# Optimization experiments

Measured on AMD Instinct MI355X. Metric: run time of the kernel, lower is better.

Reference implementation:

```python
import jax, jax.numpy as jnp
import numpy as np

N_NODES = 50000
N_EDGES = 800000
INPUT_DIM = 8
HIDDEN_DIM = 128


def setup_inputs() -> dict:
    key = jax.random.key(0)
    k = jax.random.split(key, 8)
    x = jax.random.normal(k[0], (N_NODES, INPUT_DIM), dtype=jnp.float32)
    edge_index = jax.random.randint(k[1], (2, N_EDGES), 0, N_NODES, dtype=jnp.int64)
    edge_attr = jax.random.uniform(k[2], (N_EDGES, 1), dtype=jnp.float32)
    node_embedding = jax.random.normal(k[3], (N_NODES, HIDDEN_DIM), dtype=jnp.float32)
    # Linear weights stored as [in, out] so y = x @ W (bias=False everywhere)
    s1 = 1.0 / np.sqrt(INPUT_DIM)
    sh = 1.0 / np.sqrt(HIDDEN_DIM)
    W1 = jax.random.uniform(k[4], (INPUT_DIM, HIDDEN_DIM), jnp.float32, -s1, s1)
    W2 = jax.random.uniform(k[5], (HIDDEN_DIM, HIDDEN_DIM), jnp.float32, -sh, sh)
    W3 = jax.random.uniform(k[6], (HIDDEN_DIM, HIDDEN_DIM), jnp.float32, -sh, sh)
    W4 = jax.random.uniform(k[7], (1, HIDDEN_DIM), jnp.float32, -1.0, 1.0)
    return {"x": x, "edge_index": edge_index, "edge_attr": edge_attr,
            "node_embedding": node_embedding, "W1": W1, "W2": W2, "W3": W3, "W4": W4}


def reference(x, edge_index, edge_attr, node_embedding, W1, W2, W3, W4):
    n = x.shape[0]
    row, col = edge_index[0], edge_index[1]
    # theta_1(x): [N, hidden]
    node_feature_embedding = x @ W1
    # gather neighbor embeddings along edges, scatter-sum to destination rows
    node_embedding_aggr = jax.ops.segment_sum(node_embedding[col], row, num_segments=n)
    # relu(theta_4(edge_attr)): [E, hidden], then scatter-sum to rows
    edge_feature_embedding = jax.nn.relu(edge_attr @ W4)
    edge_embedding_aggr = jax.ops.segment_sum(edge_feature_embedding, row, num_segments=n)
    return jax.nn.relu(node_feature_embedding + node_embedding_aggr @ W2 + edge_embedding_aggr @ W3)
```

## Files before the change

### kernel.cpp

```cpp
#include <hip/hip_runtime.h>

#define N_NODES 50000
#define N_EDGES 800000
#define IN_DIM  8
#define HD      128
#define N_SCAN_BLOCKS ((N_NODES + 255) / 256)
#define NREP 16
#define NTILES ((N_NODES + 63) / 64)
#define N_HIST_BLOCKS (N_EDGES / 256)
#define GRID_P1 (NTILES * 5)

typedef unsigned short ushort_t;
typedef unsigned int uint_t;
typedef __attribute__((ext_vector_type(8))) short short8;
typedef __attribute__((ext_vector_type(4))) float float4v;

static __device__ inline unsigned short f2bf(float f) {
    unsigned u = __float_as_uint(f);
    unsigned r = (u + 0x7FFF + ((u >> 16) & 1)) >> 16;
    return (unsigned short)r;
}
static __device__ inline float bf2f(unsigned short b) {
    return __uint_as_float(((unsigned)b) << 16);
}

__global__ void prep_kernel(const float* __restrict__ W2,
                            short8* __restrict__ blob) {
    int t = threadIdx.x;
#pragma unroll
    for (int i = 0; i < 8; ++i) {
        int slot = t * 8 + i;
        int f    = slot >> 6;
        int lane = slot & 63;
        int ct = f >> 2, ki = f & 3;
        int n16 = lane & 15, quad = lane >> 4;
        short8 fr;
#pragma unroll
        for (int j = 0; j < 8; ++j) {
            int k = ki * 32 + quad * 8 + j;
            fr[j] = (short)f2bf(W2[k * HD + ct * 16 + n16]);
        }
        blob[slot] = fr;
    }
}

__global__ __launch_bounds__(256, 2)
void phase1_kernel(const float* __restrict__ emb,
                   const short8* __restrict__ blob,
                   ushort_t* __restrict__ T16,
                   const int* __restrict__ ei,
                   int* __restrict__ cnt,
                   ushort_t* __restrict__ rank16) {
    __shared__ short8 sblob[2048];
    int sel = blockIdx.x % 5;

    if (sel != 0) {
        int c = (blockIdx.x / 5) * 4 + sel - 1;
        if (c >= N_HIST_BLOCKS) return;
        int e = c * 256 + threadIdx.x;
        int rep = c & (NREP - 1);
        int r = ei[e];
        int rank = atomicAdd(&cnt[rep * N_NODES + r], 1);
        rank16[e] = (ushort_t)rank;
        return;
    }

    int tt   = blockIdx.x / 5;
    int t    = threadIdx.x;
    int wave = t >> 6;
    int lane = t & 63;
    int n16  = lane & 15;
    int quad = lane >> 4;

#pragma unroll
    for (int i = 0; i < 8; ++i)
        sblob[t * 8 + i] = blob[t * 8 + i];
    __syncthreads();

    short8 bfrag[8][4];
#pragma unroll
    for (int ct = 0; ct < 8; ++ct)
#pragma unroll
        for (int ki = 0; ki < 4; ++ki)
            bfrag[ct][ki] = sblob[(ct * 4 + ki) * 64 + lane];

    int rowbase = tt * 64 + wave * 16;
    int row  = rowbase + n16;
    int rowc = row < N_NODES ? row : N_NODES - 1;
    const float4* arow = (const float4*)(emb + (size_t)rowc * HD);

    short8 afrag[4];
#pragma unroll
    for (int ki = 0; ki < 4; ++ki) {
        float4 lo = arow[ki * 8 + quad * 2];
        float4 hi = arow[ki * 8 + quad * 2 + 1];
        short8 a;
        a[0] = (short)f2bf(lo.x); a[1] = (short)f2bf(lo.y);
        a[2] = (short)f2bf(lo.z); a[3] = (short)f2bf(lo.w);
        a[4] = (short)f2bf(hi.x); a[5] = (short)f2bf(hi.y);
        a[6] = (short)f2bf(hi.z); a[7] = (short)f2bf(hi.w);
        afrag[ki] = a;
    }

    float4v acc[8];
#pragma unroll
    for (int ct = 0; ct < 8; ++ct) acc[ct] = (float4v){0.f, 0.f, 0.f, 0.f};

#pragma unroll
    for (int ki = 0; ki < 4; ++ki)
#pragma unroll
        for (int ct = 0; ct < 8; ++ct)
            acc[ct] = __builtin_amdgcn_mfma_f32_16x16x32_bf16(
                afrag[ki], bfrag[ct][ki], acc[ct], 0, 0, 0);

#pragma unroll
    for (int reg = 0; reg < 4; ++reg) {
        int r = rowbase + quad * 4 + reg;
        if (r < N_NODES) {
#pragma unroll
            for (int ct = 0; ct < 8; ++ct)
                T16[(size_t)r * HD + ct * 16 + n16] = f2bf(acc[ct][reg]);
        }
    }
}

__global__ void scan1_kernel(const int* __restrict__ cnt,
                             int* __restrict__ off,
                             int* __restrict__ bases,
                             int* __restrict__ blocksums) {
    __shared__ int lds[256];
    int t = threadIdx.x;
    int n = blockIdx.x * 256 + t;
    int c[NREP];
    int tsum = 0;
#pragma unroll
    for (int r = 0; r < NREP; ++r) {
        c[r] = (n < N_NODES) ? cnt[r * N_NODES + n] : 0;
        tsum += c[r];
    }
    lds[t] = tsum;
    __syncthreads();
    for (int o = 1; o < 256; o <<= 1) {
        int add = (t >= o) ? lds[t - o] : 0;
        __syncthreads();
        lds[t] += add;
        __syncthreads();
    }
    int ex = lds[t] - tsum;
    if (n < N_NODES) {
        off[n] = ex;
        int run = ex;
#pragma unroll
        for (int r = 0; r < NREP; ++r) {
            bases[r * N_NODES + n] = run;
            run += c[r];
        }
    }
    if (t == 255) blocksums[blockIdx.x] = lds[255];
}

__global__ void scan2_v3_kernel(int* __restrict__ blocksums,
                                const float* __restrict__ W4,
                                const float* __restrict__ W3,
                                float* __restrict__ v3) {
    int t = threadIdx.x;
    if (blockIdx.x == 1) {
        if (t < HD) {
            float acc = 0.f;
            for (int k = 0; k < HD; ++k) {
                float w = W4[k];
                w = w > 0.f ? w : 0.f;
                acc += w * W3[k * HD + t];
            }
            v3[t] = acc;
        }
        return;
    }
    __shared__ int lds[256];
    int v = (t < N_SCAN_BLOCKS) ? blocksums[t] : 0;
    lds[t] = v;
    __syncthreads();
    for (int o = 1; o < 256; o <<= 1) {
        int add = (t >= o) ? lds[t - o] : 0;
        __syncthreads();
        lds[t] += add;
        __syncthreads();
    }
    if (t < N_SCAN_BLOCKS) blocksums[t] = lds[t] - v;
}

__global__ void fill_kernel(const int* __restrict__ ei,
                            const float* __restrict__ attr,
                            const ushort_t* __restrict__ rank16,
                            const int* __restrict__ bases,
                            const int* __restrict__ bsums,
                            uint_t* __restrict__ packed) {
    int e = blockIdx.x * 256 + threadIdx.x;
    int rep = (e >> 8) & (NREP - 1);
    int r = ei[e];
    int pos = bases[rep * N_NODES + r] + bsums[r >> 8] + (int)rank16[e];
    uint_t p = ((uint_t)f2bf(attr[e]) << 16) | (uint_t)ei[N_EDGES + e];
    packed[pos] = p;
}

__global__ void aggregate_kernel(const int* __restrict__ off,
                                 const int* __restrict__ bsums,
                                 const uint_t* __restrict__ packed,
                                 const ushort_t* __restrict__ T16,
                                 const float* __restrict__ x,
                                 const float* __restrict__ W1,
                                 const float* __restrict__ v3,
                                 float* __restrict__ out) {
    int tid  = blockIdx.x * 256 + threadIdx.x;
    int node = tid >> 4;
    int lane = tid & 15;
    int s  = off[node] + bsums[node >> 8];
    int e1 = (node + 1 == N_NODES) ? N_EDGES
                                   : off[node + 1] + bsums[(node + 1) >> 8];
    int deg = e1 - s;

    float acc[8];
#pragma unroll
    for (int i = 0; i < 8; ++i) acc[i] = 0.f;
    float ssum = 0.f;

    for (int base = 0; base < deg; base += 16) {
        int rem = deg - base; if (rem > 16) rem = 16;
        uint_t p = 0;
        if (lane < rem) p = packed[s + base + lane];
        ssum += __uint_as_float(p & 0xFFFF0000u);
        int col = (int)(p & 0xFFFFu);
        int j = 0;
        for (; j + 4 <= rem; j += 4) {
            int c0 = __shfl(col, j + 0, 16);
            int c1 = __shfl(col, j + 1, 16);
            int c2 = __shfl(col, j + 2, 16);
            int c3 = __shfl(col, j + 3, 16);
            short8 t0 = ((const short8*)(T16 + (size_t)c0 * HD))[lane];
            short8 t1 = ((const short8*)(T16 + (size_t)c1 * HD))[lane];
            short8 t2 = ((const short8*)(T16 + (size_t)c2 * HD))[lane];
            short8 t3 = ((const short8*)(T16 + (size_t)c3 * HD))[lane];
#pragma unroll
            for (int i = 0; i < 8; ++i)
                acc[i] += (bf2f((ushort_t)t0[i]) + bf2f((ushort_t)t1[i]))
                        + (bf2f((ushort_t)t2[i]) + bf2f((ushort_t)t3[i]));
        }
        for (; j < rem; ++j) {
            int c = __shfl(col, j, 16);
            short8 tv = ((const short8*)(T16 + (size_t)c * HD))[lane];
#pragma unroll
            for (int i = 0; i < 8; ++i)
                acc[i] += bf2f((ushort_t)tv[i]);
        }
    }
    for (int o = 8; o; o >>= 1) ssum += __shfl_xor(ssum, o, 16);

    const float4* v3p = (const float4*)v3;
    float4 b0 = v3p[lane * 2], b1 = v3p[lane * 2 + 1];
    acc[0] += ssum * b0.x; acc[1] += ssum * b0.y;
    acc[2] += ssum * b0.z; acc[3] += ssum * b0.w;
    acc[4] += ssum * b1.x; acc[5] += ssum * b1.y;
    acc[6] += ssum * b1.z; acc[7] += ssum * b1.w;
#pragma unroll
    for (int i = 0; i < IN_DIM; ++i) {
        float xi = x[node * IN_DIM + i];
        const float4* wp = (const float4*)(W1 + i * HD);
        float4 w0 = wp[lane * 2], w1 = wp[lane * 2 + 1];
        acc[0] += xi * w0.x; acc[1] += xi * w0.y;
        acc[2] += xi * w0.z; acc[3] += xi * w0.w;
        acc[4] += xi * w1.x; acc[5] += xi * w1.y;
        acc[6] += xi * w1.z; acc[7] += xi * w1.w;
    }
    float4 o0, o1;
    o0.x = fmaxf(acc[0], 0.f); o0.y = fmaxf(acc[1], 0.f);
    o0.z = fmaxf(acc[2], 0.f); o0.w = fmaxf(acc[3], 0.f);
    o1.x = fmaxf(acc[4], 0.f); o1.y = fmaxf(acc[5], 0.f);
    o1.z = fmaxf(acc[6], 0.f); o1.w = fmaxf(acc[7], 0.f);
    float4* op = (float4*)(out + (size_t)node * HD);
    op[lane * 2]     = o0;
    op[lane * 2 + 1] = o1;
}

extern "C" void kernel_launch(void* const* d_in, const int* in_sizes, int n_in,
                              void* d_out, int out_size, void* d_ws, size_t ws_size,
                              hipStream_t stream) {
    const float* x    = (const float*)d_in[0];
    const int*   ei   = (const int*)  d_in[1];
    const float* attr = (const float*)d_in[2];
    const float* emb  = (const float*)d_in[3];
    const float* W1   = (const float*)d_in[4];
    const float* W2   = (const float*)d_in[5];
    const float* W3   = (const float*)d_in[6];
    const float* W4   = (const float*)d_in[7];
    float* out = (float*)d_out;

    char* w = (char*)d_ws;
    uint_t*   packed = (uint_t*)w;
    ushort_t* T16    = (ushort_t*)(w + (size_t)N_EDGES * 4);
    short8*   blob   = (short8*)((char*)T16 + (size_t)N_NODES * HD * 2);
    int*      off    = (int*)((char*)blob + 2048 * 16);
    int*      bases  = off + N_NODES + 4;
    int*      cnt    = bases + NREP * N_NODES;
    int*      bsums  = cnt + NREP * N_NODES;
    float*    v3     = (float*)(bsums + 256);
    ushort_t* rank16 = (ushort_t*)(v3 + HD);

    hipMemsetAsync(cnt, 0, (size_t)NREP * N_NODES * sizeof(int), stream);

    prep_kernel  <<<1, 256, 0, stream>>>(W2, blob);
    phase1_kernel<<<GRID_P1, 256, 0, stream>>>(emb, blob, T16, ei, cnt, rank16);
    scan1_kernel <<<N_SCAN_BLOCKS, 256, 0, stream>>>(cnt, off, bases, bsums);
    scan2_v3_kernel<<<2, 256, 0, stream>>>(bsums, W4, W3, v3);
    fill_kernel  <<<N_HIST_BLOCKS, 256, 0, stream>>>(ei, attr, rank16, bases, bsums, packed);
    aggregate_kernel<<<(N_NODES * 16) / 256, 256, 0, stream>>>(
        off, bsums, packed, T16, x, W1, v3, out);
}
```

Before: 191.7 us.

## Fold memset and scan2 into prep kernel, use atomic block-sum propagation

The memset is replaced by zeroing blocks inside the prep kernel, which now also computes v3. The separate scan2 kernel is removed: each scan1 block atomically adds its total into all later block offsets, so zeroing bsums alongside cnt gives exclusive prefixes. The phase1 LDS staging of the W2 fragments is dropped in favour of direct global loads, and nontemporal loads and stores are used for the embedding, packed, and output streams. This cuts two launches at the cost of O(blocks^2) atomics and uncached fragment reads.

```diff
diff --git a/kernel.cpp b/kernel.cpp
--- a/kernel.cpp
+++ b/kernel.cpp
@@ -9,11 +9,15 @@
 #define NTILES ((N_NODES + 63) / 64)
 #define N_HIST_BLOCKS (N_EDGES / 256)
 #define GRID_P1 (NTILES * 5)
+#define ZERO_INT4 ((NREP * N_NODES + 256) / 4)
+#define N_ZERO_BLOCKS ((ZERO_INT4 + 255) / 256)
+#define GRID_PREP (N_ZERO_BLOCKS + 2)
 
 typedef unsigned short ushort_t;
 typedef unsigned int uint_t;
 typedef __attribute__((ext_vector_type(8))) short short8;
 typedef __attribute__((ext_vector_type(4))) float float4v;
+typedef __attribute__((ext_vector_type(4))) int int4v;
 
 static __device__ inline unsigned short f2bf(float f) {
     unsigned u = __float_as_uint(f);
@@ -25,22 +29,47 @@
 }
 
 __global__ void prep_kernel(const float* __restrict__ W2,
-                            short8* __restrict__ blob) {
+                            short8* __restrict__ blob,
+                            int* __restrict__ cnt,
+                            const float* __restrict__ W4,
+                            const float* __restrict__ W3,
+                            float* __restrict__ v3) {
+    int b = blockIdx.x;
     int t = threadIdx.x;
-#pragma unroll
-    for (int i = 0; i < 8; ++i) {
-        int slot = t * 8 + i;
-        int f    = slot >> 6;
-        int lane = slot & 63;
-        int ct = f >> 2, ki = f & 3;
-        int n16 = lane & 15, quad = lane >> 4;
-        short8 fr;
-#pragma unroll
-        for (int j = 0; j < 8; ++j) {
-            int k = ki * 32 + quad * 8 + j;
-            fr[j] = (short)f2bf(W2[k * HD + ct * 16 + n16]);
-        }
-        blob[slot] = fr;
+    if (b < N_ZERO_BLOCKS) {
+        int idx = b * 256 + t;
+        if (idx < ZERO_INT4) {
+            int4v z = {0, 0, 0, 0};
+            ((int4v*)cnt)[idx] = z;
+        }
+        return;
+    }
+    if (b == N_ZERO_BLOCKS) {
+#pragma unroll
+        for (int i = 0; i < 8; ++i) {
+            int slot = t * 8 + i;
+            int f    = slot >> 6;
+            int lane = slot & 63;
+            int ct = f >> 2, ki = f & 3;
+            int n16 = lane & 15, quad = lane >> 4;
+            short8 fr;
+#pragma unroll
+            for (int j = 0; j < 8; ++j) {
+                int k = ki * 32 + quad * 8 + j;
+                fr[j] = (short)f2bf(W2[k * HD + ct * 16 + n16]);
+            }
+            blob[slot] = fr;
+        }
+        return;
+    }
+    if (t < HD) {
+        float acc = 0.f;
+        for (int k = 0; k < HD; ++k) {
+            float w = W4[k];
+            w = w > 0.f ? w : 0.f;
+            acc += w * W3[k * HD + t];
+        }
+        v3[t] = acc;
     }
 }
 
@@ -51,7 +80,6 @@
                    const int* __restrict__ ei,
                    int* __restrict__ cnt,
                    ushort_t* __restrict__ rank16) {
-    __shared__ short8 sblob[2048];
     int sel = blockIdx.x % 5;
 
     if (sel != 0) {
@@ -72,33 +100,28 @@
     int n16  = lane & 15;
     int quad = lane >> 4;
 
-#pragma unroll
-    for (int i = 0; i < 8; ++i)
-        sblob[t * 8 + i] = blob[t * 8 + i];
-    __syncthreads();
-
     short8 bfrag[8][4];
 #pragma unroll
     for (int ct = 0; ct < 8; ++ct)
 #pragma unroll
         for (int ki = 0; ki < 4; ++ki)
-            bfrag[ct][ki] = sblob[(ct * 4 + ki) * 64 + lane];
+            bfrag[ct][ki] = blob[(ct * 4 + ki) * 64 + lane];
 
     int rowbase = tt * 64 + wave * 16;
     int row  = rowbase + n16;
     int rowc = row < N_NODES ? row : N_NODES - 1;
-    const float4* arow = (const float4*)(emb + (size_t)rowc * HD);
+    const float4v* arow = (const float4v*)(emb + (size_t)rowc * HD);
 
     short8 afrag[4];
 #pragma unroll
     for (int ki = 0; ki < 4; ++ki) {
-        float4 lo = arow[ki * 8 + quad * 2];
-        float4 hi = arow[ki * 8 + quad * 2 + 1];
+        float4v lo = __builtin_nontemporal_load(&arow[ki * 8 + quad * 2]);
+        float4v hi = __builtin_nontemporal_load(&arow[ki * 8 + quad * 2 + 1]);
         short8 a;
-        a[0] = (short)f2bf(lo.x); a[1] = (short)f2bf(lo.y);
-        a[2] = (short)f2bf(lo.z); a[3] = (short)f2bf(lo.w);
-        a[4] = (short)f2bf(hi.x); a[5] = (short)f2bf(hi.y);
-        a[6] = (short)f2bf(hi.z); a[7] = (short)f2bf(hi.w);
+        a[0] = (short)f2bf(lo[0]); a[1] = (short)f2bf(lo[1]);
+        a[2] = (short)f2bf(lo[2]); a[3] = (short)f2bf(lo[3]);
+        a[4] = (short)f2bf(hi[0]); a[5] = (short)f2bf(hi[1]);
+        a[6] = (short)f2bf(hi[2]); a[7] = (short)f2bf(hi[3]);
         afrag[ki] = a;
     }
 
@@ -127,7 +150,7 @@
 __global__ void scan1_kernel(const int* __restrict__ cnt,
                              int* __restrict__ off,
                              int* __restrict__ bases,
-                             int* __restrict__ blocksums) {
+                             int* __restrict__ bsums) {
     __shared__ int lds[256];
     int t = threadIdx.x;
     int n = blockIdx.x * 256 + t;
@@ -147,6 +170,7 @@
         __syncthreads();
     }
     int ex = lds[t] - tsum;
+    int total = lds[255];
     if (n < N_NODES) {
         off[n] = ex;
         int run = ex;
@@ -156,37 +180,8 @@
             run += c[r];
         }
     }
-    if (t == 255) blocksums[blockIdx.x] = lds[255];
-}
-
-__global__ void scan2_v3_kernel(int* __restrict__ blocksums,
-                                const float* __restrict__ W4,
-                                const float* __restrict__ W3,
-                                float* __restrict__ v3) {
-    int t = threadIdx.x;
-    if (blockIdx.x == 1) {
-        if (t < HD) {
-            float acc = 0.f;
-            for (int k = 0; k < HD; ++k) {
-                float w = W4[k];
-                w = w > 0.f ? w : 0.f;
-                acc += w * W3[k * HD + t];
-            }
-            v3[t] = acc;
-        }
-        return;
-    }
-    __shared__ int lds[256];
-    int v = (t < N_SCAN_BLOCKS) ? blocksums[t] : 0;
-    lds[t] = v;
-    __syncthreads();
-    for (int o = 1; o < 256; o <<= 1) {
-        int add = (t >= o) ? lds[t - o] : 0;
-        __syncthreads();
-        lds[t] += add;
-        __syncthreads();
-    }
-    if (t < N_SCAN_BLOCKS) blocksums[t] = lds[t] - v;
+    for (int bb = blockIdx.x + 1 + t; bb < N_SCAN_BLOCKS; bb += 256)
+        atomicAdd(&bsums[bb], total);
 }
 
 __global__ void fill_kernel(const int* __restrict__ ei,
@@ -227,7 +222,7 @@
     for (int base = 0; base < deg; base += 16) {
         int rem = deg - base; if (rem > 16) rem = 16;
         uint_t p = 0;
-        if (lane < rem) p = packed[s + base + lane];
+        if (lane < rem) p = __builtin_nontemporal_load(&packed[s + base + lane]);
         ssum += __uint_as_float(p & 0xFFFF0000u);
         int col = (int)(p & 0xFFFFu);
         int j = 0;
@@ -255,30 +250,30 @@
     }
     for (int o = 8; o; o >>= 1) ssum += __shfl_xor(ssum, o, 16);
 
-    const float4* v3p = (const float4*)v3;
-    float4 b0 = v3p[lane * 2], b1 = v3p[lane * 2 + 1];
-    acc[0] += ssum * b0.x; acc[1] += ssum * b0.y;
-    acc[2] += ssum * b0.z; acc[3] += ssum * b0.w;
-    acc[4] += ssum * b1.x; acc[5] += ssum * b1.y;
-    acc[6] += ssum * b1.z; acc[7] += ssum * b1.w;
+    const float4v* v3p = (const float4v*)v3;
+    float4v b0 = v3p[lane * 2], b1 = v3p[lane * 2 + 1];
+    acc[0] += ssum * b0[0]; acc[1] += ssum * b0[1];
+    acc[2] += ssum * b0[2]; acc[3] += ssum * b0[3];
+    acc[4] += ssum * b1[0]; acc[5] += ssum * b1[1];
+    acc[6] += ssum * b1[2]; acc[7] += ssum * b1[3];
 #pragma unroll
     for (int i = 0; i < IN_DIM; ++i) {
         float xi = x[node * IN_DIM + i];
-        const float4* wp = (const float4*)(W1 + i * HD);
-        float4 w0 = wp[lane * 2], w1 = wp[lane * 2 + 1];
-        acc[0] += xi * w0.x; acc[1] += xi * w0.y;
-        acc[2] += xi * w0.z; acc[3] += xi * w0.w;
-        acc[4] += xi * w1.x; acc[5] += xi * w1.y;
-        acc[6] += xi * w1.z; acc[7] += xi * w1.w;
-    }
-    float4 o0, o1;
-    o0.x = fmaxf(acc[0], 0.f); o0.y = fmaxf(acc[1], 0.f);
-    o0.z = fmaxf(acc[2], 0.f); o0.w = fmaxf(acc[3], 0.f);
-    o1.x = fmaxf(acc[4], 0.f); o1.y = fmaxf(acc[5], 0.f);
-    o1.z = fmaxf(acc[6], 0.f); o1.w = fmaxf(acc[7], 0.f);
-    float4* op = (float4*)(out + (size_t)node * HD);
-    op[lane * 2]     = o0;
-    op[lane * 2 + 1] = o1;
+        const float4v* wp = (const float4v*)(W1 + i * HD);
+        float4v w0 = wp[lane * 2], w1 = wp[lane * 2 + 1];
+        acc[0] += xi * w0[0]; acc[1] += xi * w0[1];
+        acc[2] += xi * w0[2]; acc[3] += xi * w0[3];
+        acc[4] += xi * w1[0]; acc[5] += xi * w1[1];
+        acc[6] += xi * w1[2]; acc[7] += xi * w1[3];
+    }
+    float4v o0, o1;
+    o0[0] = fmaxf(acc[0], 0.f); o0[1] = fmaxf(acc[1], 0.f);
+    o0[2] = fmaxf(acc[2], 0.f); o0[3] = fmaxf(acc[3], 0.f);
+    o1[0] = fmaxf(acc[4], 0.f); o1[1] = fmaxf(acc[5], 0.f);
+    o1[2] = fmaxf(acc[6], 0.f); o1[3] = fmaxf(acc[7], 0.f);
+    float4v* op = (float4v*)(out + (size_t)node * HD);
+    __builtin_nontemporal_store(o0, op + lane * 2);
+    __builtin_nontemporal_store(o1, op + lane * 2 + 1);
 }
 
 extern "C" void kernel_launch(void* const* d_in, const int* in_sizes, int n_in,
@@ -305,12 +300,9 @@
     float*    v3     = (float*)(bsums + 256);
     ushort_t* rank16 = (ushort_t*)(v3 + HD);
 
-    hipMemsetAsync(cnt, 0, (size_t)NREP * N_NODES * sizeof(int), stream);
-
-    prep_kernel  <<<1, 256, 0, stream>>>(W2, blob);
+    prep_kernel  <<<GRID_PREP, 256, 0, stream>>>(W2, blob, cnt, W4, W3, v3);
     phase1_kernel<<<GRID_P1, 256, 0, stream>>>(emb, blob, T16, ei, cnt, rank16);
     scan1_kernel <<<N_SCAN_BLOCKS, 256, 0, stream>>>(cnt, off, bases, bsums);
-    scan2_v3_kernel<<<2, 256, 0, stream>>>(bsums, W4, W3, v3);
     fill_kernel  <<<N_HIST_BLOCKS, 256, 0, stream>>>(ei, attr, rank16, bases, bsums, packed);
     aggregate_kernel<<<(N_NODES * 16) / 256, 256, 0, stream>>>(
         off, bsums, packed, T16, x, W1, v3, out);
```

After: 195.7 us. 2.1% more time.
